# Kernel optimization log

Hardware: AMD Instinct MI355X
Metric: run time of the kernel (lower is better)

The kernel has to match this reference:

```python
import jax, jax.numpy as jnp
import numpy as np

C = 256
CR = C // 4  # channel_attention_reduce=4


def _dw(x, w, b, ph, pw):
    # depthwise conv, NCHW, kernel w: (C,1,kh,kw)
    y = jax.lax.conv_general_dilated(
        x, w, (1, 1), ((ph, ph), (pw, pw)),
        dimension_numbers=("NCHW", "OIHW", "NCHW"),
        feature_group_count=x.shape[1])
    return y + b[None, :, None, None]


def _conv1x1(x, w, b):
    # w: (Cout, Cin)
    return jnp.einsum("bchw,oc->bohw", x, w) + b[None, :, None, None]


def _channel_att(x, fc1_w, fc1_b, fc2_w, fc2_b):
    def branch(p):  # p: (B, C)
        h = jax.nn.relu(p @ fc1_w.T + fc1_b)
        return jax.nn.sigmoid(h @ fc2_w.T + fc2_b)
    avg = jnp.mean(x, axis=(2, 3))
    mx = jnp.max(x, axis=(2, 3))
    att = branch(avg) + branch(mx)  # (B, C)
    return att[:, :, None, None]


def setup_inputs() -> dict:
    key = jax.random.key(0)
    ks = jax.random.split(key, 24)
    s = 0.05
    d = {
        "x": jax.random.normal(ks[0], (16, C, 56, 56), jnp.float32),
        "conv_w": jax.random.normal(ks[1], (C, C), jnp.float32) * s,
        "conv_b": jax.random.normal(ks[2], (C,), jnp.float32) * s,
        "fc1_w": jax.random.normal(ks[3], (CR, C), jnp.float32) * s,
        "fc1_b": jax.random.normal(ks[4], (CR,), jnp.float32) * s,
        "fc2_w": jax.random.normal(ks[5], (C, CR), jnp.float32) * s,
        "fc2_b": jax.random.normal(ks[6], (C,), jnp.float32) * s,
        "dw5x5_w": jax.random.normal(ks[7], (C, 1, 5, 5), jnp.float32) * s,
        "dw5x5_b": jax.random.normal(ks[8], (C,), jnp.float32) * s,
        "dw1x7_w": jax.random.normal(ks[9], (C, 1, 1, 7), jnp.float32) * s,
        "dw1x7_b": jax.random.normal(ks[10], (C,), jnp.float32) * s,
        "dw7x1_w": jax.random.normal(ks[11], (C, 1, 7, 1), jnp.float32) * s,
        "dw7x1_b": jax.random.normal(ks[12], (C,), jnp.float32) * s,
        "dw1x11_w": jax.random.normal(ks[13], (C, 1, 1, 11), jnp.float32) * s,
        "dw1x11_b": jax.random.normal(ks[14], (C,), jnp.float32) * s,
        "dw11x1_w": jax.random.normal(ks[15], (C, 1, 11, 1), jnp.float32) * s,
        "dw11x1_b": jax.random.normal(ks[16], (C,), jnp.float32) * s,
        "dw1x21_w": jax.random.normal(ks[17], (C, 1, 1, 21), jnp.float32) * s,
        "dw1x21_b": jax.random.normal(ks[18], (C,), jnp.float32) * s,
        "dw21x1_w": jax.random.normal(ks[19], (C, 1, 21, 1), jnp.float32) * s,
        "dw21x1_b": jax.random.normal(ks[20], (C,), jnp.float32) * s,
    }
    return d


def reference(x, conv_w, conv_b, fc1_w, fc1_b, fc2_w, fc2_b,
              dw5x5_w, dw5x5_b, dw1x7_w, dw1x7_b, dw7x1_w, dw7x1_b,
              dw1x11_w, dw1x11_b, dw11x1_w, dw11x1_b,
              dw1x21_w, dw1x21_b, dw21x1_w, dw21x1_b):
    h = jax.nn.gelu(_conv1x1(x, conv_w, conv_b), approximate=False)
    h = _channel_att(h, fc1_w, fc1_b, fc2_w, fc2_b) * h
    x_init = _dw(h, dw5x5_w, dw5x5_b, 2, 2)
    x1 = _dw(_dw(x_init, dw1x7_w, dw1x7_b, 0, 3), dw7x1_w, dw7x1_b, 3, 0)
    x2 = _dw(_dw(x_init, dw1x11_w, dw1x11_b, 0, 5), dw11x1_w, dw11x1_b, 5, 0)
    x3 = _dw(_dw(x_init, dw1x21_w, dw1x21_b, 0, 10), dw21x1_w, dw21x1_b, 10, 0)
    xs = x_init + x1 + x2 + x3
    spatial_att = _conv1x1(xs, conv_w, conv_b)
    out = spatial_att * h
    return _conv1x1(out, conv_w, conv_b)
```

## Files before the change

### kernel.cpp

```cpp
#include <hip/hip_runtime.h>
#include <hip/hip_bf16.h>

#define HW 3136
#define NB 16

typedef float f32x4 __attribute__((ext_vector_type(4)));
typedef short short8 __attribute__((ext_vector_type(8)));
typedef unsigned short ushort8 __attribute__((ext_vector_type(8)));

__device__ inline unsigned short bfb(float f) {
  union { __hip_bfloat16 h; unsigned short u; } cv;
  cv.h = __float2bfloat16(f);
  return cv.u;
}
__device__ inline unsigned pack2(float lo, float hi) {
  return (unsigned)bfb(lo) | ((unsigned)bfb(hi) << 16);
}
__device__ inline unsigned fenc(float f) {
  unsigned u = __float_as_uint(f);
  return (u & 0x80000000u) ? ~u : (u | 0x80000000u);
}
__device__ inline float fdec(unsigned e) {
  return (e & 0x80000000u) ? __uint_as_float(e & 0x7FFFFFFFu) : __uint_as_float(~e);
}
__device__ inline float bf2f(unsigned short u) {
  return __uint_as_float((unsigned)u << 16);
}

__global__ __launch_bounds__(256) void k0_init(const float* __restrict__ conv_w,
                                               unsigned short* __restrict__ Wbf,
                                               float* __restrict__ psum,
                                               unsigned* __restrict__ pmaxe) {
  int i = blockIdx.x * 256 + threadIdx.x;
  Wbf[i] = bfb(conv_w[i]);
  if (i < 4096) psum[i] = 0.f;
  else if (i < 8192) pmaxe[i - 4096] = 0u;
}

__global__ __launch_bounds__(256) void k1_conv_gelu_pool(
    const float* __restrict__ x, const unsigned short* __restrict__ Wbf,
    const float* __restrict__ conv_b, unsigned short* __restrict__ h_out,
    float* __restrict__ psum, unsigned* __restrict__ pmaxe)
{
  __shared__ __align__(16) unsigned short Bs[64 * 264];
  const int bid = blockIdx.x;
  const int b = bid / 49, tile = bid - 49 * (bid / 49);
  const int hw0 = tile * 64;
  const int t = threadIdx.x;

  {
    int g = t & 127, half = t >> 7;
    const float* p0 = x + ((size_t)(b * 256 + 2 * g)) * HW + hw0 + half * 32;
    const float* p1 = p0 + HW;
    unsigned* Bd = (unsigned*)Bs;
#pragma unroll
    for (int i = 0; i < 32; i += 4) {
      float4 a4 = *(const float4*)(p0 + i);
      float4 c4 = *(const float4*)(p1 + i);
      int hw = half * 32 + i;
      Bd[(hw + 0) * 132 + g] = pack2(a4.x, c4.x);
      Bd[(hw + 1) * 132 + g] = pack2(a4.y, c4.y);
      Bd[(hw + 2) * 132 + g] = pack2(a4.z, c4.z);
      Bd[(hw + 3) * 132 + g] = pack2(a4.w, c4.w);
    }
  }
  __syncthreads();

  const int w = t >> 6, l = t & 63, hq = l & 15, g2 = l >> 4;
  const int wm0 = w * 64;
  const f32x4 vzero = {0.f, 0.f, 0.f, 0.f};
  f32x4 acc[4][4];
#pragma unroll
  for (int mi = 0; mi < 4; ++mi)
#pragma unroll
    for (int ni = 0; ni < 4; ++ni) acc[mi][ni] = vzero;

#pragma unroll
  for (int ks = 0; ks < 8; ++ks) {
    short8 a[4], bv[4];
#pragma unroll
    for (int mi = 0; mi < 4; ++mi)
      a[mi] = *(const short8*)(Wbf + (size_t)(wm0 + mi * 16 + hq) * 256 + ks * 32 + g2 * 8);
#pragma unroll
    for (int ni = 0; ni < 4; ++ni)
      bv[ni] = *(const short8*)(Bs + (ni * 16 + hq) * 264 + ks * 32 + g2 * 8);
#pragma unroll
    for (int mi = 0; mi < 4; ++mi)
#pragma unroll
      for (int ni = 0; ni < 4; ++ni)
        acc[mi][ni] = __builtin_amdgcn_mfma_f32_16x16x32_bf16(a[mi], bv[ni], acc[mi][ni], 0, 0, 0);
  }
  __syncthreads();

#pragma unroll
  for (int mi = 0; mi < 4; ++mi) {
#pragma unroll
    for (int r = 0; r < 4; ++r) {
      int o = wm0 + mi * 16 + g2 * 4 + r;
      float bias = conv_b[o];
#pragma unroll
      for (int ni = 0; ni < 4; ++ni) {
        float s = acc[mi][ni][r] + bias;
        float v = 0.5f * s * (1.0f + erff(s * 0.70710678118654752f));
        Bs[(ni * 16 + hq) * 264 + o] = bfb(v);
      }
    }
  }
  __syncthreads();

  {
    const int o = t;
    float sm = 0.f, mx = -1e30f;
    unsigned pk[32];
#pragma unroll
    for (int m = 0; m < 32; ++m) {
      unsigned short r0 = Bs[(2 * m) * 264 + o];
      unsigned short r1 = Bs[(2 * m + 1) * 264 + o];
      float f0 = bf2f(r0), f1 = bf2f(r1);
      sm += f0 + f1;
      mx = fmaxf(mx, fmaxf(f0, f1));
      pk[m] = (unsigned)r0 | ((unsigned)r1 << 16);
    }
    unsigned short* hp = h_out + ((size_t)(b * 256 + o)) * HW + hw0;
#pragma unroll
    for (int q = 0; q < 8; ++q) {
      uint4 s4;
      s4.x = pk[q * 4 + 0]; s4.y = pk[q * 4 + 1]; s4.z = pk[q * 4 + 2]; s4.w = pk[q * 4 + 3];
      *(uint4*)(hp + q * 8) = s4;
    }
    atomicAdd(psum + b * 256 + o, sm);
    atomicMax(pmaxe + b * 256 + o, fenc(mx));
  }
}

__global__ __launch_bounds__(256) void k2_att(
    const float* __restrict__ psum, const unsigned* __restrict__ pmaxe,
    const float* __restrict__ fc1_w, const float* __restrict__ fc1_b,
    const float* __restrict__ fc2_w, const float* __restrict__ fc2_b,
    float* __restrict__ att)
{
  const int b = blockIdx.x, t = threadIdx.x;
  __shared__ float pA[4][64], pM[4][64];
  __shared__ float hA[64], hM[64];
  {
    const int j = t & 63, seg = t >> 6;
    const int base = b * 256 + seg * 64;
    const float* wrow = fc1_w + j * 256 + seg * 64;
    float sA = 0.f, sM = 0.f;
#pragma unroll 8
    for (int c = 0; c < 64; ++c) {
      float wv = wrow[c];
      sA += psum[base + c] * wv;
      sM += fdec(pmaxe[base + c]) * wv;
    }
    pA[seg][j] = sA;
    pM[seg][j] = sM;
  }
  __syncthreads();
  if (t < 64) {
    float a = fc1_b[t] + (pA[0][t] + pA[1][t] + pA[2][t] + pA[3][t]) * (1.f / 3136.f);
    float m = fc1_b[t] + (pM[0][t] + pM[1][t] + pM[2][t] + pM[3][t]);
    hA[t] = fmaxf(a, 0.f);
    hM[t] = fmaxf(m, 0.f);
  }
  __syncthreads();
  float s1 = fc2_b[t], s2 = s1;
#pragma unroll 8
  for (int j = 0; j < 64; ++j) {
    float wv = fc2_w[t * 64 + j];
    s1 += hA[j] * wv;
    s2 += hM[j] * wv;
  }
  att[b * 256 + t] = 1.f / (1.f + expf(-s1)) + 1.f / (1.f + expf(-s2));
}

__global__ __launch_bounds__(256) void k34_dw(
    const unsigned short* __restrict__ h_in, const float* __restrict__ att,
    const float* __restrict__ w5, const float* __restrict__ b5,
    const float* __restrict__ w1x7, const float* __restrict__ b1x7,
    const float* __restrict__ w7x1, const float* __restrict__ b7x1,
    const float* __restrict__ w1x11, const float* __restrict__ b1x11,
    const float* __restrict__ w11x1, const float* __restrict__ b11x1,
    const float* __restrict__ w1x21, const float* __restrict__ b1x21,
    const float* __restrict__ w21x1, const float* __restrict__ b21x1,
    unsigned short* __restrict__ xs_out)
{
  __shared__ __align__(16) float B0[4256];
  __shared__ __align__(16) unsigned short T1[62 * 56];
  __shared__ __align__(16) unsigned short T2[66 * 56];
  __shared__ __align__(16) unsigned short T3[76 * 56];
  __shared__ __align__(16) float wk5a[25];
  __shared__ __align__(16) float wk[78];

  const int bid = blockIdx.x;
  const int b = bid >> 8, c = bid & 255;
  const int t = threadIdx.x;
  const size_t plane = (size_t)(b * 256 + c) * HW;
  const float a = att[b * 256 + c];

  if (t < 25) wk5a[t] = w5[c * 25 + t] * a;
  if (t >= 32 && t < 110) {
    int k = t - 32;
    float v;
    if (k < 7) v = w1x7[c * 7 + k];
    else if (k < 14) v = w7x1[c * 7 + k - 7];
    else if (k < 25) v = w1x11[c * 11 + k - 14];
    else if (k < 36) v = w11x1[c * 11 + k - 25];
    else if (k < 57) v = w1x21[c * 21 + k - 36];
    else v = w21x1[c * 21 + k - 57];
    wk[k] = v;
  }
  {
    unsigned* T1d = (unsigned*)T1; unsigned* T2d = (unsigned*)T2; unsigned* T3d = (unsigned*)T3;
    for (int i = t; i < 1008; i += 256) {
      if (i < 84) T1d[i] = 0;
      else if (i < 168) T1d[1652 + i - 84] = 0;
      else if (i < 308) T2d[i - 168] = 0;
      else if (i < 448) T2d[1708 + i - 308] = 0;
      else if (i < 728) T3d[i - 448] = 0;
      else T3d[1848 + i - 728] = 0;
    }
  }
  {
    const unsigned short* hp = h_in + plane;
    for (int idx = t; idx < 3600; idx += 256) {
      int ly = idx / 60, lx = idx - ly * 60;
      int gy = ly - 2, gx = lx - 2;
      float v = 0.f;
      if ((unsigned)gy < 56u && (unsigned)gx < 56u) v = bf2f(hp[gy * 56 + gx]);
      B0[idx] = v;
    }
  }
  __syncthreads();

  float xv0[8], xv1[8];
  const float bias5 = b5[c];
  {
    int tau = t, yq = tau / 56, xx = tau - yq * 56, y0 = yq * 8;
    float accv[8];
#pragma unroll
    for (int d = 0; d < 8; ++d) accv[d] = bias5;
#pragma unroll
    for (int kx = 0; kx < 5; ++kx) {
      float col[12];
#pragma unroll
      for (int ry = 0; ry < 12; ++ry) col[ry] = B0[(y0 + ry) * 60 + xx + kx];
#pragma unroll
      for (int ky = 0; ky < 5; ++ky) {
        float wv = wk5a[ky * 5 + kx];
#pragma unroll
        for (int d = 0; d < 8; ++d) accv[d] += col[d + ky] * wv;
      }
    }
#pragma unroll
    for (int d = 0; d < 8; ++d) xv0[d] = accv[d];
  }
  if (t < 136) {
    int tau = t + 256, yq = tau / 56, xx = tau - yq * 56, y0 = yq * 8;
    float accv[8];
#pragma unroll
    for (int d = 0; d < 8; ++d) accv[d] = bias5;
#pragma unroll
    for (int kx = 0; kx < 5; ++kx) {
      float col[12];
#pragma unroll
      for (int ry = 0; ry < 12; ++ry) col[ry] = B0[(y0 + ry) * 60 + xx + kx];
#pragma unroll
      for (int ky = 0; ky < 5; ++ky) {
        float wv = wk5a[ky * 5 + kx];
#pragma unroll
        for (int d = 0; d < 8; ++d) accv[d] += col[d + ky] * wv;
      }
    }
#pragma unroll
    for (int d = 0; d < 8; ++d) xv1[d] = accv[d];
  }
  __syncthreads();

  {
    int tau = t, yq = tau / 56, xx = tau - yq * 56, y0 = yq * 8;
#pragma unroll
    for (int d = 0; d < 8; ++d) B0[(y0 + d) * 76 + 10 + xx] = xv0[d];
  }
  if (t < 136) {
    int tau = t + 256, yq = tau / 56, xx = tau - yq * 56, y0 = yq * 8;
#pragma unroll
    for (int d = 0; d < 8; ++d) B0[(y0 + d) * 76 + 10 + xx] = xv1[d];
  }
  for (int i = t; i < 1120; i += 256) {
    int y = i / 20, j = i - y * 20;
    int lx = (j < 10) ? j : (56 + j);
    B0[y * 76 + lx] = 0.f;
  }
  __syncthreads();

  const float bb1 = b1x7[c], bb2 = b1x11[c], bb3 = b1x21[c];
#pragma unroll
  for (int rnd = 0; rnd < 2; ++rnd) {
    if (rnd == 1 && t >= 136) break;
    int tau = t + rnd * 256;
    int y = tau / 7, x0 = (tau - y * 7) * 8;
    float win[28];
    const float* rp = B0 + y * 76 + x0;
#pragma unroll
    for (int j = 0; j < 28; j += 4) {
      float4 q = *(const float4*)(rp + j);
      win[j] = q.x; win[j + 1] = q.y; win[j + 2] = q.z; win[j + 3] = q.w;
    }
    float o1[8], o2[8], o3[8];
#pragma unroll
    for (int d = 0; d < 8; ++d) { o1[d] = bb1; o2[d] = bb2; o3[d] = bb3; }
#pragma unroll
    for (int k = 0; k < 7; ++k) {
      float wv = wk[k];
#pragma unroll
      for (int d = 0; d < 8; ++d) o1[d] += win[d + k + 7] * wv;
    }
#pragma unroll
    for (int k = 0; k < 11; ++k) {
      float wv = wk[14 + k];
#pragma unroll
      for (int d = 0; d < 8; ++d) o2[d] += win[d + k + 5] * wv;
    }
#pragma unroll
    for (int k = 0; k < 21; ++k) {
      float wv = wk[36 + k];
#pragma unroll
      for (int d = 0; d < 8; ++d) o3[d] += win[d + k] * wv;
    }
    uint4 s1, s2, s3;
    s1.x = pack2(o1[0], o1[1]); s1.y = pack2(o1[2], o1[3]); s1.z = pack2(o1[4], o1[5]); s1.w = pack2(o1[6], o1[7]);
    s2.x = pack2(o2[0], o2[1]); s2.y = pack2(o2[2], o2[3]); s2.z = pack2(o2[4], o2[5]); s2.w = pack2(o2[6], o2[7]);
    s3.x = pack2(o3[0], o3[1]); s3.y = pack2(o3[2], o3[3]); s3.z = pack2(o3[4], o3[5]); s3.w = pack2(o3[6], o3[7]);
    *(uint4*)&T1[(y + 3) * 56 + x0] = s1;
    *(uint4*)&T2[(y + 5) * 56 + x0] = s2;
    *(uint4*)&T3[(y + 10) * 56 + x0] = s3;
  }
  __syncthreads();

  const float vb = b7x1[c] + b11x1[c] + b21x1[c];
  unsigned short* op = xs_out + plane;
  if (t < 196) {
    int band = t / 28, xp = t - band * 28;
    int y0 = band * 8, x0 = xp * 2;
    float rlo[8], rhi[8];
#pragma unroll
    for (int d = 0; d < 8; ++d) {
      float2 q = *(const float2*)&B0[(y0 + d) * 76 + 10 + x0];
      rlo[d] = q.x + vb; rhi[d] = q.y + vb;
    }
    {
      float clo[14], chi[14];
#pragma unroll
      for (int j = 0; j < 14; ++j) {
        unsigned q = *(const unsigned*)&T1[(y0 + j) * 56 + x0];
        clo[j] = __uint_as_float(q << 16);
        chi[j] = __uint_as_float(q & 0xffff0000u);
      }
#pragma unroll
      for (int k = 0; k < 7; ++k) {
        float wv = wk[7 + k];
#pragma unroll
        for (int d = 0; d < 8; ++d) { rlo[d] += clo[d + k] * wv; rhi[d] += chi[d + k] * wv; }
      }
    }
    {
      float clo[18], chi[18];
#pragma unroll
      for (int j = 0; j < 18; ++j) {
        unsigned q = *(const unsigned*)&T2[(y0 + j) * 56 + x0];
        clo[j] = __uint_as_float(q << 16);
        chi[j] = __uint_as_float(q & 0xffff0000u);
      }
#pragma unroll
      for (int k = 0; k < 11; ++k) {
        float wv = wk[25 + k];
#pragma unroll
        for (int d = 0; d < 8; ++d) { rlo[d] += clo[d + k] * wv; rhi[d] += chi[d + k] * wv; }
      }
    }
    {
      float clo[28], chi[28];
#pragma unroll
      for (int j = 0; j < 28; ++j) {
        unsigned q = *(const unsigned*)&T3[(y0 + j) * 56 + x0];
        clo[j] = __uint_as_float(q << 16);
        chi[j] = __uint_as_float(q & 0xffff0000u);
      }
#pragma unroll
      for (int k = 0; k < 21; ++k) {
        float wv = wk[57 + k];
#pragma unroll
        for (int d = 0; d < 8; ++d) { rlo[d] += clo[d + k] * wv; rhi[d] += chi[d + k] * wv; }
      }
    }
#pragma unroll
    for (int d = 0; d < 8; ++d)
      *(unsigned*)&op[(y0 + d) * 56 + x0] = pack2(rlo[d], rhi[d]);
  }
}

__global__ __launch_bounds__(256) void k5_final(
    const unsigned short* __restrict__ xs, const unsigned short* __restrict__ Wbf,
    const float* __restrict__ conv_b, const float* __restrict__ att,
    const unsigned short* __restrict__ h_in, float* __restrict__ outp)
{
  __shared__ __align__(16) unsigned short Bs[64 * 264];
  const int bid = blockIdx.x;
  const int b = bid / 49, tile = bid - 49 * (bid / 49);
  const int hw0 = tile * 64;
  const int t = threadIdx.x;

  {
    int g = t & 127, half = t >> 7;
    const unsigned short* p0 = xs + ((size_t)(b * 256 + 2 * g)) * HW + hw0 + half * 32;
    const unsigned short* p1 = p0 + HW;
    unsigned* Bd = (unsigned*)Bs;
#pragma unroll
    for (int i = 0; i < 32; i += 8) {
      ushort8 a8 = *(const ushort8*)(p0 + i);
      ushort8 c8 = *(const ushort8*)(p1 + i);
      int hw = half * 32 + i;
#pragma unroll
      for (int e = 0; e < 8; ++e)
        Bd[(hw + e) * 132 + g] = (unsigned)a8[e] | ((unsigned)c8[e] << 16);
    }
  }
  __syncthreads();

  const int w = t >> 6, l = t & 63, hq = l & 15, g2 = l >> 4;
  const int wm0 = w * 64;
  const f32x4 vzero = {0.f, 0.f, 0.f, 0.f};
  f32x4 acc[4][4];
#pragma unroll
  for (int mi = 0; mi < 4; ++mi)
#pragma unroll
    for (int ni = 0; ni < 4; ++ni) acc[mi][ni] = vzero;

#pragma unroll
  for (int ks = 0; ks < 8; ++ks) {
    short8 a[4], bv[4];
#pragma unroll
    for (int mi = 0; mi < 4; ++mi)
      a[mi] = *(const short8*)(Wbf + (size_t)(wm0 + mi * 16 + hq) * 256 + ks * 32 + g2 * 8);
#pragma unroll
    for (int ni = 0; ni < 4; ++ni)
      bv[ni] = *(const short8*)(Bs + (ni * 16 + hq) * 264 + ks * 32 + g2 * 8);
#pragma unroll
    for (int mi = 0; mi < 4; ++mi)
#pragma unroll
      for (int ni = 0; ni < 4; ++ni)
        acc[mi][ni] = __builtin_amdgcn_mfma_f32_16x16x32_bf16(a[mi], bv[ni], acc[mi][ni], 0, 0, 0);
  }
  __syncthreads();

#pragma unroll
  for (int mi = 0; mi < 4; ++mi) {
#pragma unroll
    for (int r = 0; r < 4; ++r) {
      int o = wm0 + mi * 16 + g2 * 4 + r;
      float bias = conv_b[o];
      float av = att[b * 256 + o];
      const unsigned short* hp = h_in + ((size_t)(b * 256 + o)) * HW + hw0;
#pragma unroll
      for (int ni = 0; ni < 4; ++ni) {
        float sa = acc[mi][ni][r] + bias;
        float ov = sa * (av * bf2f(hp[ni * 16 + hq]));
        Bs[(ni * 16 + hq) * 264 + o] = bfb(ov);
      }
    }
  }
  __syncthreads();

  f32x4 acc2[4][4];
#pragma unroll
  for (int mi = 0; mi < 4; ++mi)
#pragma unroll
    for (int ni = 0; ni < 4; ++ni) acc2[mi][ni] = vzero;
#pragma unroll
  for (int ks = 0; ks < 8; ++ks) {
    short8 a[4], bv[4];
#pragma unroll
    for (int mi = 0; mi < 4; ++mi)
      a[mi] = *(const short8*)(Wbf + (size_t)(wm0 + mi * 16 + hq) * 256 + ks * 32 + g2 * 8);
#pragma unroll
    for (int ni = 0; ni < 4; ++ni)
      bv[ni] = *(const short8*)(Bs + (ni * 16 + hq) * 264 + ks * 32 + g2 * 8);
#pragma unroll
    for (int mi = 0; mi < 4; ++mi)
#pragma unroll
      for (int ni = 0; ni < 4; ++ni)
        acc2[mi][ni] = __builtin_amdgcn_mfma_f32_16x16x32_bf16(a[mi], bv[ni], acc2[mi][ni], 0, 0, 0);
  }

#pragma unroll
  for (int mi = 0; mi < 4; ++mi) {
#pragma unroll
    for (int r = 0; r < 4; ++r) {
      int o = wm0 + mi * 16 + g2 * 4 + r;
      float bias = conv_b[o];
      float* op = outp + ((size_t)(b * 256 + o)) * HW + hw0;
#pragma unroll
      for (int ni = 0; ni < 4; ++ni) op[ni * 16 + hq] = acc2[mi][ni][r] + bias;
    }
  }
}

extern "C" void kernel_launch(void* const* d_in, const int* in_sizes, int n_in,
                              void* d_out, int out_size, void* d_ws, size_t ws_size,
                              hipStream_t stream) {
  const float* x      = (const float*)d_in[0];
  const float* conv_w = (const float*)d_in[1];
  const float* conv_b = (const float*)d_in[2];
  const float* fc1_w  = (const float*)d_in[3];
  const float* fc1_b  = (const float*)d_in[4];
  const float* fc2_w  = (const float*)d_in[5];
  const float* fc2_b  = (const float*)d_in[6];
  const float* w5     = (const float*)d_in[7];
  const float* b5     = (const float*)d_in[8];
  const float* w1x7   = (const float*)d_in[9];
  const float* b1x7   = (const float*)d_in[10];
  const float* w7x1   = (const float*)d_in[11];
  const float* b7x1   = (const float*)d_in[12];
  const float* w1x11  = (const float*)d_in[13];
  const float* b1x11  = (const float*)d_in[14];
  const float* w11x1  = (const float*)d_in[15];
  const float* b11x1  = (const float*)d_in[16];
  const float* w1x21  = (const float*)d_in[17];
  const float* b1x21  = (const float*)d_in[18];
  const float* w21x1  = (const float*)d_in[19];
  const float* b21x1  = (const float*)d_in[20];
  float* out = (float*)d_out;

  char* ws = (char*)d_ws;
  unsigned short* Wbf = (unsigned short*)(ws);
  float* psum   = (float*)(ws + 131072);
  unsigned* pme = (unsigned*)(ws + 147456);
  float* attb   = (float*)(ws + 163840);
  unsigned short* hbuf = (unsigned short*)(ws + 180224);
  unsigned short* xbuf = (unsigned short*)(ws + 180224 + 25690112);

  k0_init<<<256, 256, 0, stream>>>(conv_w, Wbf, psum, pme);
  k1_conv_gelu_pool<<<784, 256, 0, stream>>>(x, Wbf, conv_b, hbuf, psum, pme);
  k2_att<<<16, 256, 0, stream>>>(psum, pme, fc1_w, fc1_b, fc2_w, fc2_b, attb);
  k34_dw<<<4096, 256, 0, stream>>>(hbuf, attb, w5, b5, w1x7, b1x7, w7x1, b7x1,
                                   w1x11, b1x11, w11x1, b11x1, w1x21, b1x21,
                                   w21x1, b21x1, xbuf);
  k5_final<<<784, 256, 0, stream>>>(xbuf, Wbf, conv_b, attb, hbuf, out);
}
```

Measured before the change: 204.3 us.

## Remap 5x5 depthwise to 2-wide pixel tiles and keep results in registers

The 5x5 depthwise stage now uses the same 8-row by 2-column tile per thread as the final vertical stage. It runs on 196 threads with packed 2-wide float math instead of 392 single-column work items split across two rounds. Because each thread owns the same pixels in both stages, the x_init values stay in registers and are reused directly in the final sum, so they no longer have to be read back from shared memory. This aims to cut LDS traffic and make packed FMA possible. In exchange, the stage uses fewer active threads and more registers stay live across the middle section.

Result: faster. 186.3 us (-8.8%).

```diff
diff --git a/kernel.cpp b/kernel.cpp
--- a/kernel.cpp
+++ b/kernel.cpp
@@ -5,6 +5,7 @@
 #define NB 16
 
 typedef float f32x4 __attribute__((ext_vector_type(4)));
+typedef float f32x2 __attribute__((ext_vector_type(2)));
 typedef short short8 __attribute__((ext_vector_type(8)));
 typedef unsigned short ushort8 __attribute__((ext_vector_type(8)));
 
@@ -233,59 +234,41 @@
   }
   __syncthreads();
 
-  float xv0[8], xv1[8];
-  const float bias5 = b5[c];
-  {
-    int tau = t, yq = tau / 56, xx = tau - yq * 56, y0 = yq * 8;
-    float accv[8];
-#pragma unroll
-    for (int d = 0; d < 8; ++d) accv[d] = bias5;
-#pragma unroll
-    for (int kx = 0; kx < 5; ++kx) {
-      float col[12];
-#pragma unroll
-      for (int ry = 0; ry < 12; ++ry) col[ry] = B0[(y0 + ry) * 60 + xx + kx];
-#pragma unroll
-      for (int ky = 0; ky < 5; ++ky) {
-        float wv = wk5a[ky * 5 + kx];
-#pragma unroll
-        for (int d = 0; d < 8; ++d) accv[d] += col[d + ky] * wv;
-      }
-    }
-#pragma unroll
-    for (int d = 0; d < 8; ++d) xv0[d] = accv[d];
-  }
-  if (t < 136) {
-    int tau = t + 256, yq = tau / 56, xx = tau - yq * 56, y0 = yq * 8;
-    float accv[8];
-#pragma unroll
-    for (int d = 0; d < 8; ++d) accv[d] = bias5;
-#pragma unroll
-    for (int kx = 0; kx < 5; ++kx) {
-      float col[12];
-#pragma unroll
-      for (int ry = 0; ry < 12; ++ry) col[ry] = B0[(y0 + ry) * 60 + xx + kx];
-#pragma unroll
-      for (int ky = 0; ky < 5; ++ky) {
-        float wv = wk5a[ky * 5 + kx];
-#pragma unroll
-        for (int d = 0; d < 8; ++d) accv[d] += col[d + ky] * wv;
-      }
-    }
-#pragma unroll
-    for (int d = 0; d < 8; ++d) xv1[d] = accv[d];
-  }
-  __syncthreads();
-
-  {
-    int tau = t, yq = tau / 56, xx = tau - yq * 56, y0 = yq * 8;
-#pragma unroll
-    for (int d = 0; d < 8; ++d) B0[(y0 + d) * 76 + 10 + xx] = xv0[d];
-  }
-  if (t < 136) {
-    int tau = t + 256, yq = tau / 56, xx = tau - yq * 56, y0 = yq * 8;
-#pragma unroll
-    for (int d = 0; d < 8; ++d) B0[(y0 + d) * 76 + 10 + xx] = xv1[d];
+  const int band = t / 28, xp = t - band * 28;
+  const int py0 = band * 8, px0 = xp * 2;
+  f32x2 acc2[8];
+  {
+    const float bias5 = b5[c];
+#pragma unroll
+    for (int d = 0; d < 8; ++d) { acc2[d].x = bias5; acc2[d].y = bias5; }
+  }
+  if (t < 196) {
+#pragma unroll
+    for (int r = 0; r < 12; ++r) {
+      float row6[6];
+#pragma unroll
+      for (int k6 = 0; k6 < 6; ++k6) row6[k6] = B0[(py0 + r) * 60 + px0 + k6];
+      const int dlo = (r > 4) ? (r - 4) : 0;
+      const int dhi = (r < 7) ? r : 7;
+#pragma unroll
+      for (int d = 0; d < 8; ++d) {
+        if (d < dlo || d > dhi) continue;
+        const int ky = r - d;
+#pragma unroll
+        for (int kx = 0; kx < 5; ++kx) {
+          float wv = wk5a[ky * 5 + kx];
+          f32x2 p; p.x = row6[kx]; p.y = row6[kx + 1];
+          acc2[d] = acc2[d] + p * wv;
+        }
+      }
+    }
+  }
+  __syncthreads();
+
+  if (t < 196) {
+#pragma unroll
+    for (int d = 0; d < 8; ++d)
+      *(f32x2*)&B0[(py0 + d) * 76 + 10 + px0] = acc2[d];
   }
   for (int i = t; i < 1120; i += 256) {
     int y = i / 20, j = i - y * 20;
@@ -341,62 +324,57 @@
   const float vb = b7x1[c] + b11x1[c] + b21x1[c];
   unsigned short* op = xs_out + plane;
   if (t < 196) {
-    int band = t / 28, xp = t - band * 28;
-    int y0 = band * 8, x0 = xp * 2;
-    float rlo[8], rhi[8];
-#pragma unroll
-    for (int d = 0; d < 8; ++d) {
-      float2 q = *(const float2*)&B0[(y0 + d) * 76 + 10 + x0];
-      rlo[d] = q.x + vb; rhi[d] = q.y + vb;
-    }
+    f32x2 r2[8];
+#pragma unroll
+    for (int d = 0; d < 8; ++d) r2[d] = acc2[d] + vb;
     {
-      float clo[14], chi[14];
+      f32x2 c2[14];
 #pragma unroll
       for (int j = 0; j < 14; ++j) {
-        unsigned q = *(const unsigned*)&T1[(y0 + j) * 56 + x0];
-        clo[j] = __uint_as_float(q << 16);
-        chi[j] = __uint_as_float(q & 0xffff0000u);
+        unsigned q = *(const unsigned*)&T1[(py0 + j) * 56 + px0];
+        c2[j].x = __uint_as_float(q << 16);
+        c2[j].y = __uint_as_float(q & 0xffff0000u);
       }
 #pragma unroll
       for (int k = 0; k < 7; ++k) {
         float wv = wk[7 + k];
 #pragma unroll
-        for (int d = 0; d < 8; ++d) { rlo[d] += clo[d + k] * wv; rhi[d] += chi[d + k] * wv; }
+        for (int d = 0; d < 8; ++d) r2[d] = r2[d] + c2[d + k] * wv;
       }
     }
     {
-      float clo[18], chi[18];
+      f32x2 c2[18];
 #pragma unroll
       for (int j = 0; j < 18; ++j) {
-        unsigned q = *(const unsigned*)&T2[(y0 + j) * 56 + x0];
-        clo[j] = __uint_as_float(q << 16);
-        chi[j] = __uint_as_float(q & 0xffff0000u);
+        unsigned q = *(const unsigned*)&T2[(py0 + j) * 56 + px0];
+        c2[j].x = __uint_as_float(q << 16);
+        c2[j].y = __uint_as_float(q & 0xffff0000u);
       }
 #pragma unroll
       for (int k = 0; k < 11; ++k) {
         float wv = wk[25 + k];
 #pragma unroll
-        for (int d = 0; d < 8; ++d) { rlo[d] += clo[d + k] * wv; rhi[d] += chi[d + k] * wv; }
+        for (int d = 0; d < 8; ++d) r2[d] = r2[d] + c2[d + k] * wv;
       }
     }
     {
-      float clo[28], chi[28];
+      f32x2 c2[28];
 #pragma unroll
       for (int j = 0; j < 28; ++j) {
-        unsigned q = *(const unsigned*)&T3[(y0 + j) * 56 + x0];
-        clo[j] = __uint_as_float(q << 16);
-        chi[j] = __uint_as_float(q & 0xffff0000u);
+        unsigned q = *(const unsigned*)&T3[(py0 + j) * 56 + px0];
+        c2[j].x = __uint_as_float(q << 16);
+        c2[j].y = __uint_as_float(q & 0xffff0000u);
       }
 #pragma unroll
       for (int k = 0; k < 21; ++k) {
         float wv = wk[57 + k];
 #pragma unroll
-        for (int d = 0; d < 8; ++d) { rlo[d] += clo[d + k] * wv; rhi[d] += chi[d + k] * wv; }
+        for (int d = 0; d < 8; ++d) r2[d] = r2[d] + c2[d + k] * wv;
       }
     }
 #pragma unroll
     for (int d = 0; d < 8; ++d)
-      *(unsigned*)&op[(y0 + d) * 56 + x0] = pack2(rlo[d], rhi[d]);
+      *(unsigned*)&op[(py0 + d) * 56 + px0] = pack2(r2[d].x, r2[d].y);
   }
 }
 
```
